# Performance work log

Measured on AMD Instinct MI355X. Metric: run time of the kernel, lower is better.

Reference implementation:

```python
import jax, jax.numpy as jnp
import numpy as np

B = 8
C = 256
N40, N20, N10 = 1600, 400, 100
N = N40 + N20 + N10  # 2100 pixel nodes (40x40 + 20x20 + 10x10)

def _grid_edges(h, w, off):
    # 8-neighborhood 'contextual' edges within one scale's grid
    idx = np.arange(h * w).reshape(h, w)
    srcs, dsts = [], []
    for di in (-1, 0, 1):
        for dj in (-1, 0, 1):
            if di == 0 and dj == 0:
                continue
            s = idx[max(0, -di):h - max(0, di), max(0, -dj):w - max(0, dj)]
            d = idx[max(0, di):h - max(0, -di), max(0, dj):w - max(0, -dj)]
            srcs.append(off + s.ravel())
            dsts.append(off + d.ravel())
    return srcs, dsts

def _hier_edges(ph, pw, poff, coff):
    # bidirected parent <-> 4-children 'hierarchical' edges between scales
    i, j = np.meshgrid(np.arange(ph), np.arange(pw), indexing='ij')
    parent = (poff + i * pw + j).ravel()
    srcs, dsts = [], []
    cw = 2 * pw
    for di in (0, 1):
        for dj in (0, 1):
            child = (coff + (2 * i + di) * cw + (2 * j + dj)).ravel()
            srcs += [parent, child]
            dsts += [child, parent]
    return srcs, dsts

def build_edges():
    loop = [np.arange(N)]  # dgl.add_self_loop on both etypes
    cs, cd = [], []
    for (h, w, off) in ((40, 40, 0), (20, 20, N40), (10, 10, N40 + N20)):
        s, d = _grid_edges(h, w, off)
        cs += s; cd += d
    ctx_src = np.concatenate(cs + loop); ctx_dst = np.concatenate(cd + loop)
    hs, hd = [], []
    s, d = _hier_edges(20, 20, N40, 0); hs += s; hd += d
    s, d = _hier_edges(10, 10, N40 + N20, N40); hs += s; hd += d
    hier_src = np.concatenate(hs + loop); hier_dst = np.concatenate(hd + loop)
    return (jnp.asarray(ctx_src, jnp.int32), jnp.asarray(ctx_dst, jnp.int32),
            jnp.asarray(hier_src, jnp.int32), jnp.asarray(hier_dst, jnp.int32))

def _bn_relu(x, g, b, m, v):
    # inference-mode BatchNorm2d + ReLU
    scale = g * jax.lax.rsqrt(v + 1e-5)
    return jax.nn.relu(x * scale[:, None, None] + (b - m * scale)[:, None, None])

def _conv1x1(x, w, b):
    return jnp.einsum('bchw,oc->bohw', x, w) + b[:, None, None]

def _avgpool2(x):
    b, c, h, w = x.shape
    return x.reshape(b, c, h // 2, 2, w // 2, 2).mean(axis=(3, 5))

def _up2(x):
    return jnp.repeat(jnp.repeat(x, 2, axis=2), 2, axis=3)

def _gnn(h, src, dst, deg_inv, w, b):
    # gather -> scatter-add -> mean over in-neighbors (incl. self loop) -> linear -> ReLU
    agg = jnp.zeros_like(h).at[:, dst].add(h[:, src]) * deg_inv[None, :, None]
    return jax.nn.relu(jnp.einsum('bnc,cd->bnd', agg, w) + b)

def _convT2x2(x, wt, b):
    # stride-2 2x2 transposed conv; wt: [Cin, Cout, 2, 2] (torch layout)
    bsz, cin, h, w = x.shape
    y = jnp.einsum('bchw,cokl->bohkwl', x, wt)
    return y.reshape(bsz, wt.shape[1], 2 * h, 2 * w) + b[:, None, None]

def setup_inputs():
    key = jax.random.key(0)
    ks = iter(jax.random.split(key, 64))
    def rn(shape, scale=0.02):
        return jax.random.normal(next(ks), shape, jnp.float32) * scale
    inp = {}
    inp['feat0'] = rn((B, 256, 160, 160), 1.0)
    inp['feat1'] = rn((B, 512, 80, 80), 1.0)
    inp['feat2'] = rn((B, 1024, 40, 40), 1.0)
    inp['feat3'] = rn((B, 2048, 20, 20), 1.0)
    for i, cin in ((1, 512), (2, 1024), (3, 2048)):
        inp['dw%d' % i] = rn((256, cin))
        inp['db%d' % i] = jnp.zeros((256,), jnp.float32)
        inp['g%d' % i] = jnp.ones((256,), jnp.float32)
        inp['b%d' % i] = jnp.zeros((256,), jnp.float32)
        inp['m%d' % i] = jnp.zeros((256,), jnp.float32)
        inp['v%d' % i] = jnp.ones((256,), jnp.float32)
    for i in range(1, 7):
        inp['gW%d' % i] = rn((256, 256))
        inp['gb%d' % i] = jnp.zeros((256,), jnp.float32)
    for i, cout in ((1, 512), (2, 1024), (3, 2048)):
        inp['tW%d' % i] = rn((256, cout, 2, 2))
        inp['tb%d' % i] = jnp.zeros((cout,), jnp.float32)
    ctx_src, ctx_dst, hier_src, hier_dst = build_edges()
    inp['ctx_src'] = ctx_src; inp['ctx_dst'] = ctx_dst
    inp['hier_src'] = hier_src; inp['hier_dst'] = hier_dst
    return inp

def reference(feat0, feat1, feat2, feat3,
              dw1, db1, g1, b1, m1, v1,
              dw2, db2, g2, b2, m2, v2,
              dw3, db3, g3, b3, m3, v3,
              gW1, gb1, gW2, gb2, gW3, gb3, gW4, gb4, gW5, gb5, gW6, gb6,
              tW1, tb1, tW2, tb2, tW3, tb3,
              ctx_src, ctx_dst, hier_src, hier_dst):
    f40 = _avgpool2(_bn_relu(_conv1x1(feat1, dw1, db1), g1, b1, m1, v1))  # [B,256,40,40]
    f20 = _avgpool2(_bn_relu(_conv1x1(feat2, dw2, db2), g2, b2, m2, v2))  # [B,256,20,20]
    f10 = _avgpool2(_bn_relu(_conv1x1(feat3, dw3, db3), g3, b3, m3, v3))  # [B,256,10,10]
    bsz = f40.shape[0]
    # cnn_gnn: flatten all three scales into [B, 2100, 256] node features (batched
    # version of the original per-sample python loop; graph is identical per sample)
    h = jnp.concatenate([
        f40.reshape(bsz, C, N40).transpose(0, 2, 1),
        f20.reshape(bsz, C, N20).transpose(0, 2, 1),
        f10.reshape(bsz, C, N10).transpose(0, 2, 1)], axis=1)
    dic = 1.0 / jnp.zeros((N,), h.dtype).at[ctx_dst].add(1.0)
    dih = 1.0 / jnp.zeros((N,), h.dtype).at[hier_dst].add(1.0)
    # context1, context2, hierarch1, hierarch2, context4, context5
    h = _gnn(h, ctx_src, ctx_dst, dic, gW1, gb1)
    h = _gnn(h, ctx_src, ctx_dst, dic, gW2, gb2)
    h = _gnn(h, hier_src, hier_dst, dih, gW3, gb3)
    h = _gnn(h, hier_src, hier_dst, dih, gW4, gb4)
    h = _gnn(h, ctx_src, ctx_dst, dic, gW5, gb5)
    h = _gnn(h, ctx_src, ctx_dst, dic, gW6, gb6)
    # gnn_cnn: split back to NCHW maps
    f40g = h[:, :N40].transpose(0, 2, 1).reshape(bsz, C, 40, 40)
    f20g = h[:, N40:N40 + N20].transpose(0, 2, 1).reshape(bsz, C, 20, 20)
    f10g = h[:, N40 + N20:].transpose(0, 2, 1).reshape(bsz, C, 10, 10)
    f10_ref = f10 + f10g
    f20_ref = f20 + f20g + _up2(f10g)
    f40_ref = f40 + f40g + _up2(f20g)
    out1 = _convT2x2(f40_ref, tW1, tb1) + feat1
    out2 = _convT2x2(f20_ref, tW2, tb2) + feat2
    out3 = _convT2x2(f10_ref, tW3, tb3) + feat3
    return (feat0, out1, out2, out3)
```

## Files before the change

kernel.cpp:

```cpp
#include <hip/hip_runtime.h>
#include <cstdint>

#define NODES 2100

typedef __attribute__((ext_vector_type(8))) __bf16 bf16x8;
typedef __attribute__((ext_vector_type(4))) float f32x4;
typedef __attribute__((ext_vector_type(8))) unsigned short u16x8;

__device__ inline float bf2f(unsigned short s) { return __uint_as_float(((unsigned)s) << 16); }
__device__ inline unsigned short f2bf(float f) {
    unsigned u = __float_as_uint(f);
    u += 0x7fff + ((u >> 16) & 1);
    return (unsigned short)(u >> 16);
}
__device__ inline void gload16(const unsigned short* g, void* lds) {
    __builtin_amdgcn_global_load_lds(
        (const __attribute__((address_space(1))) void*)g,
        (__attribute__((address_space(3))) void*)lds, 16, 0, 0);
}

struct PrepArgs {
    const float *dw0, *dw1, *dw2;
    const float *gw0, *gw1, *gw2, *gw3, *gw4, *gw5;
    const float *tw0, *tw1, *tw2;
    const float *g0, *g1, *g2, *b0, *b1, *b2, *m0, *m1, *m2, *v0, *v1, *v2, *db0, *db1, *db2;
    unsigned short *dwb, *gWTb, *tWTb;
    float *scshb;
};

__device__ inline void transpose32(const float* __restrict__ in, unsigned short* __restrict__ outT,
                                   int Ccols, int c0, int r0)
{
    __shared__ float T[32][33];
    const int tx = threadIdx.x & 31, ty = threadIdx.x >> 5;
#pragma unroll
    for (int i = 0; i < 4; ++i)
        T[ty + i * 8][tx] = in[(size_t)(r0 + ty + i * 8) * Ccols + c0 + tx];
    __syncthreads();
#pragma unroll
    for (int i = 0; i < 4; ++i)
        outT[(size_t)(c0 + ty + i * 8) * 256 + r0 + tx] = f2bf(T[tx][ty + i * 8]);
}

__global__ __launch_bounds__(256)
void mega_prep(PrepArgs a)
{
    int bid = blockIdx.x;
    const int t = threadIdx.x;
    if (bid < 448) {
        int idx = (bid * 256 + t) * 8;
        const float* src;
        int loc;
        if (idx < 131072)      { src = a.dw0; loc = idx; }
        else if (idx < 393216) { src = a.dw1; loc = idx - 131072; }
        else                   { src = a.dw2; loc = idx - 393216; }
        float4 x = *(const float4*)(src + loc);
        float4 y = *(const float4*)(src + loc + 4);
        u16x8 r;
        r[0] = f2bf(x.x); r[1] = f2bf(x.y); r[2] = f2bf(x.z); r[3] = f2bf(x.w);
        r[4] = f2bf(y.x); r[5] = f2bf(y.y); r[6] = f2bf(y.z); r[7] = f2bf(y.w);
        *(u16x8*)(a.dwb + idx) = r;
    } else if (bid < 832) {
        int gid = bid - 448;
        int l = gid >> 6, sb = gid & 63;
        const float* gw[6] = {a.gw0, a.gw1, a.gw2, a.gw3, a.gw4, a.gw5};
        transpose32(gw[l], a.gWTb + (size_t)l * 65536, 256, (sb & 7) << 5, (sb >> 3) << 5);
    } else if (bid < 4416) {
        int gid = bid - 832;
        const float* tw; unsigned short* dst; int ncx, loc;
        if (gid < 512)       { tw = a.tw0; dst = a.tWTb;           ncx = 64;  loc = gid; }
        else if (gid < 1536) { tw = a.tw1; dst = a.tWTb + 524288;  ncx = 128; loc = gid - 512; }
        else                 { tw = a.tw2; dst = a.tWTb + 1572864; ncx = 256; loc = gid - 1536; }
        int cx = loc % ncx, ry = loc / ncx;
        transpose32(tw, dst, ncx * 32, cx << 5, ry << 5);
    } else {
        const float* g[3]  = {a.g0, a.g1, a.g2};
        const float* b[3]  = {a.b0, a.b1, a.b2};
        const float* m[3]  = {a.m0, a.m1, a.m2};
        const float* v[3]  = {a.v0, a.v1, a.v2};
        const float* db[3] = {a.db0, a.db1, a.db2};
        for (int s = 0; s < 3; ++s) {
            float sc = g[s][t] * rsqrtf(v[s][t] + 1e-5f);
            a.scshb[s * 512 + t] = sc;
            a.scshb[s * 512 + 256 + t] = (db[s][t] - m[s][t]) * sc + b[s][t];
        }
    }
}

struct ConvArgs {
    const float* feat[3];
    const unsigned short* dwb[3];
    const float* scsh[3];
    unsigned short* h0out;
};

__global__ __launch_bounds__(256)
void conv_fused(ConvArgs ca)
{
    __shared__ __align__(16) unsigned short As[64 * 64];
    __shared__ __align__(16) unsigned short Bs[256 * 64];
    int bx = blockIdx.x;
    int s, mt;
    if (bx < 800)       { s = 0; mt = bx; }
    else if (bx < 1000) { s = 1; mt = bx - 800; }
    else                { s = 2; mt = bx - 1000; }
    const int Kc[3]  = {512, 1024, 2048};
    const int Wc[3]  = {80, 40, 20};
    const int PPc[3] = {1600, 400, 100};
    const int nfc[3] = {0, 1600, 2000};
    const int K = Kc[s], W = Wc[s], W2 = W >> 1, HW = W * W, PP = PPc[s], noff = nfc[s];
    const float* feat = ca.feat[s];
    const unsigned short* dw = ca.dwb[s];
    const float* scsh = ca.scsh[s];

    const int t = threadIdx.x, lane = t & 63, w = t >> 6;
    const int sx = (lane & 7) << 4;

    const int ml = t & 63;
    const int kw = t >> 6;
    const int graw = mt * 64 + ml;
    const int b = graw / HW;
    const int rem = graw - b * HW;
    const int pooled = rem >> 2, sub = rem & 3;
    const int pi = pooled / W2, pj = pooled - pi * W2;
    const int i = pi * 2 + (sub >> 1), j = pj * 2 + (sub & 1);
    const float* src = feat + (size_t)b * K * HW + (size_t)i * W + j;
    const int sxm = (ml & 7) << 3;

    f32x4 acc[4][4];
#pragma unroll
    for (int fr = 0; fr < 4; ++fr)
#pragma unroll
        for (int fc = 0; fc < 4; ++fc) acc[fr][fc] = (f32x4){0.f, 0.f, 0.f, 0.f};

    for (int k0 = 0; k0 < K; k0 += 64) {
#pragma unroll
        for (int it = 0; it < 8; ++it) {
            int LO = ((it << 8) + t) << 4;
            int row = LO >> 7;
            int kb = (LO & 127) ^ ((row & 7) << 4);
            gload16(dw + (size_t)row * K + k0 + (kb >> 1), (char*)Bs + LO);
        }
        float v[16];
#pragma unroll
        for (int it = 0; it < 16; ++it)
            v[it] = src[(size_t)(k0 + it * 4 + kw) * HW];
#pragma unroll
        for (int it = 0; it < 16; ++it) {
            int k_l = it * 4 + kw;
            As[(ml << 6) + (k_l ^ sxm)] = f2bf(v[it]);
        }
        asm volatile("s_waitcnt vmcnt(0)" ::: "memory");
        __syncthreads();
#pragma unroll
        for (int kk = 0; kk < 2; ++kk) {
            bf16x8 a[4], bb[4];
#pragma unroll
            for (int f = 0; f < 4; ++f) {
                int pa = (((f * 16 + (lane & 15)) << 7) + kk * 64 + ((lane >> 4) << 4)) ^ sx;
                int pb = (((w * 64 + f * 16 + (lane & 15)) << 7) + kk * 64 + ((lane >> 4) << 4)) ^ sx;
                a[f]  = *(const bf16x8*)((const char*)As + pa);
                bb[f] = *(const bf16x8*)((const char*)Bs + pb);
            }
#pragma unroll
            for (int fr = 0; fr < 4; ++fr)
#pragma unroll
                for (int fc = 0; fc < 4; ++fc)
                    acc[fr][fc] = __builtin_amdgcn_mfma_f32_16x16x32_bf16(a[fr], bb[fc], acc[fr][fc], 0, 0, 0);
        }
        __syncthreads();
    }

#pragma unroll
    for (int fc = 0; fc < 4; ++fc) {
        const int o = w * 64 + fc * 16 + (lane & 15);
        const float sc = scsh[o], sh = scsh[256 + o];
#pragma unroll
        for (int fr = 0; fr < 4; ++fr) {
            const int mrow = mt * 64 + fr * 16 + (lane >> 4) * 4;
            const int q = mrow >> 2;
            const int bi = q / PP;
            const int node = noff + (q - bi * PP);
            float sum = 0.f;
#pragma unroll
            for (int r = 0; r < 4; ++r)
                sum += fmaxf(acc[fr][fc][r] * sc + sh, 0.f);
            ca.h0out[((size_t)(bi * NODES + node)) * 256 + o] = f2bf(sum * 0.25f);
        }
    }
}

__global__ __launch_bounds__(256)
void gnn_fused(const unsigned short* __restrict__ h, const unsigned short* __restrict__ BT,
               const float* __restrict__ bias, unsigned short* __restrict__ out, int hier)
{
    __shared__ __align__(16) unsigned short As[32 * 64];
    __shared__ __align__(16) unsigned short Bs[256 * 64];
    const int t = threadIdx.x, lane = t & 63, w = t >> 6;
    const int r0 = blockIdx.x << 5;
    const int myrow = t >> 3, q = t & 7;
    const int grow = r0 + myrow;
    const int b = grow / NODES;
    const int n = grow - b * NODES;

    int gw, off;
    if (n < 1600)      { gw = 40; off = 0; }
    else if (n < 2000) { gw = 20; off = 1600; }
    else               { gw = 10; off = 2000; }
    const int li = (n - off) / gw;
    const int lj = (n - off) - li * gw;
    int nbr[9]; int cnt = 0;
    if (!hier) {
#pragma unroll
        for (int di = -1; di <= 1; ++di)
#pragma unroll
            for (int dj = -1; dj <= 1; ++dj) {
                int ii = li + di, jj = lj + dj;
                if (ii >= 0 && ii < gw && jj >= 0 && jj < gw) nbr[cnt++] = off + ii * gw + jj;
            }
    } else {
        nbr[cnt++] = n;
        if (off == 0) {
            nbr[cnt++] = 1600 + (li >> 1) * 20 + (lj >> 1);
        } else if (off == 1600) {
            nbr[cnt++] = 2000 + (li >> 1) * 10 + (lj >> 1);
#pragma unroll
            for (int di = 0; di < 2; ++di)
#pragma unroll
                for (int dj = 0; dj < 2; ++dj)
                    nbr[cnt++] = ((li << 1) + di) * 40 + ((lj << 1) + dj);
        } else {
#pragma unroll
            for (int di = 0; di < 2; ++di)
#pragma unroll
                for (int dj = 0; dj < 2; ++dj)
                    nbr[cnt++] = 1600 + ((li << 1) + di) * 20 + ((lj << 1) + dj);
        }
    }
    int nboff[9];
#pragma unroll
    for (int e = 0; e < 9; ++e)
        nboff[e] = (b * NODES + nbr[e < cnt ? e : 0]) * 256 + q * 8;
    const float inv = 1.0f / (float)cnt;
    const int sx = (lane & 7) << 4;
    const int awr = (myrow << 6) + ((q ^ (myrow & 7)) << 3);

    f32x4 acc[2][4];
#pragma unroll
    for (int fr = 0; fr < 2; ++fr)
#pragma unroll
        for (int fc = 0; fc < 4; ++fc) acc[fr][fc] = (f32x4){0.f, 0.f, 0.f, 0.f};

    u16x8 pre[9];
#pragma unroll
    for (int e = 0; e < 9; ++e) pre[e] = *(const u16x8*)(h + nboff[e]);

    for (int k0 = 0; k0 < 256; k0 += 64) {
#pragma unroll
        for (int it = 0; it < 8; ++it) {
            int LO = ((it << 8) + t) << 4;
            int row = LO >> 7;
            int kb = (LO & 127) ^ ((row & 7) << 4);
            gload16(BT + (size_t)row * 256 + k0 + (kb >> 1), (char*)Bs + LO);
        }
        float sacc[8] = {0, 0, 0, 0, 0, 0, 0, 0};
#pragma unroll
        for (int e = 0; e < 9; ++e) {
            if (e < cnt) {
#pragma unroll
                for (int jj = 0; jj < 8; ++jj) sacc[jj] += bf2f(pre[e][jj]);
            }
        }
        u16x8 o0;
#pragma unroll
        for (int jj = 0; jj < 8; ++jj) o0[jj] = f2bf(sacc[jj] * inv);
        *(u16x8*)&As[awr] = o0;

        asm volatile("s_waitcnt vmcnt(0)" ::: "memory");
        __syncthreads();

        const int k0n = (k0 + 64) & 255;
#pragma unroll
        for (int e = 0; e < 9; ++e) pre[e] = *(const u16x8*)(h + nboff[e] + k0n);

#pragma unroll
        for (int kk = 0; kk < 2; ++kk) {
            bf16x8 a[2], bb[4];
#pragma unroll
            for (int f = 0; f < 2; ++f) {
                int pa = (((f * 16 + (lane & 15)) << 7) + kk * 64 + ((lane >> 4) << 4)) ^ sx;
                a[f] = *(const bf16x8*)((const char*)As + pa);
            }
#pragma unroll
            for (int f = 0; f < 4; ++f) {
                int pb = (((w * 64 + f * 16 + (lane & 15)) << 7) + kk * 64 + ((lane >> 4) << 4)) ^ sx;
                bb[f] = *(const bf16x8*)((const char*)Bs + pb);
            }
#pragma unroll
            for (int fr = 0; fr < 2; ++fr)
#pragma unroll
                for (int fc = 0; fc < 4; ++fc)
                    acc[fr][fc] = __builtin_amdgcn_mfma_f32_16x16x32_bf16(a[fr], bb[fc], acc[fr][fc], 0, 0, 0);
        }
        __syncthreads();
    }

#pragma unroll
    for (int fc = 0; fc < 4; ++fc) {
        const int d = w * 64 + fc * 16 + (lane & 15);
        const float bv = bias[d];
#pragma unroll
        for (int fr = 0; fr < 2; ++fr) {
            int rb = r0 + fr * 16 + (lane >> 4) * 4;
#pragma unroll
            for (int r = 0; r < 4; ++r)
                out[(size_t)(rb + r) * 256 + d] = f2bf(fmaxf(acc[fr][fc][r] + bv, 0.f));
        }
    }
}

__global__ __launch_bounds__(256)
void a_build(const unsigned short* __restrict__ h0, const unsigned short* __restrict__ h6,
             unsigned short* __restrict__ Ao)
{
    int bx = blockIdx.x;
    int P, H2, noff, pbase, pw, haspar; size_t aoff;
    if (bx < 1600)      { P = 1600; H2 = 40; noff = 0;    pbase = 1600; pw = 20; haspar = 1; aoff = 0; }
    else if (bx < 2000) { P = 400;  H2 = 20; noff = 1600; pbase = 2000; pw = 10; haspar = 1; aoff = 12800ULL * 256; bx -= 1600; }
    else                { P = 100;  H2 = 10; noff = 2000; pbase = 0;    pw = 0;  haspar = 0; aoff = 16000ULL * 256; bx -= 2000; }
    const int gid = bx * 256 + threadIdx.x;
    const int m = gid >> 5, c0 = (gid & 31) << 3;
    const int b = m / P, pix = m - b * P;
    const size_t src = ((size_t)(b * NODES + noff + pix)) * 256 + c0;
    u16x8 x0 = *(const u16x8*)(h0 + src);
    u16x8 x6 = *(const u16x8*)(h6 + src);
    float v[8];
#pragma unroll
    for (int e = 0; e < 8; ++e) v[e] = bf2f(x0[e]) + bf2f(x6[e]);
    if (haspar) {
        int ii = pix / H2, jj = pix - ii * H2;
        size_t sp = ((size_t)(b * NODES + pbase + (ii >> 1) * pw + (jj >> 1))) * 256 + c0;
        u16x8 xp = *(const u16x8*)(h6 + sp);
#pragma unroll
        for (int e = 0; e < 8; ++e) v[e] += bf2f(xp[e]);
    }
    u16x8 r;
#pragma unroll
    for (int e = 0; e < 8; ++e) r[e] = f2bf(v[e]);
    *(u16x8*)(Ao + aoff + (size_t)m * 256 + c0) = r;
}

struct ConvtArgs {
    const unsigned short* WT[3];
    const unsigned short* Apix[3];
    const float* tb[3];
    const float* feat[3];
    float* out[3];
    const float4* cps; float4* cpd;
};

__global__ __launch_bounds__(256)
void convt_fused(ConvtArgs ct)
{
    __shared__ __align__(16) unsigned short As[4096], Bs[4096];
    int bx = blockIdx.x;
    if (bx < 1024) {
        const int base = bx * 256 + threadIdx.x;
        const int stride = 1024 * 256;
        const float4* s = ct.cps;
        float4* d = ct.cpd;
        for (int j = 0; j < 50; j += 5) {
            float4 v0 = s[base + (size_t)(j + 0) * stride];
            float4 v1 = s[base + (size_t)(j + 1) * stride];
            float4 v2 = s[base + (size_t)(j + 2) * stride];
            float4 v3 = s[base + (size_t)(j + 3) * stride];
            float4 v4 = s[base + (size_t)(j + 4) * stride];
            d[base + (size_t)(j + 0) * stride] = v0;
            d[base + (size_t)(j + 1) * stride] = v1;
            d[base + (size_t)(j + 2) * stride] = v2;
            d[base + (size_t)(j + 3) * stride] = v3;
            d[base + (size_t)(j + 4) * stride] = v4;
        }
        return;
    }
    bx -= 1024;
    int s, px, my;
    if (bx < 6400)      { s = 0; px = bx >> 5; my = bx & 31; }
    else if (bx < 9600) { s = 1; bx -= 6400; px = bx >> 6; my = bx & 63; }
    else                { s = 2; bx -= 9600; px = bx >> 7; my = bx & 127; }
    const int Pc[3]  = {1600, 400, 100};
    const int H2c[3] = {40, 20, 10};
    const int Cc[3]  = {512, 1024, 2048};
    const int Mc[3]  = {12800, 3200, 800};
    const int P = Pc[s], H2 = H2c[s], Cout = Cc[s], Mpix = Mc[s];
    const int m0 = my << 6, n0 = px << 6;
    const unsigned short* WT = ct.WT[s];
    const unsigned short* Apix = ct.Apix[s];
    const int nClamp = Mpix - 1;

    const int t = threadIdx.x, lane = t & 63, w = t >> 6;
    const int wr = w >> 1, wc = w & 1;
    const int sx = (lane & 7) << 4;

    f32x4 acc[2][2];
#pragma unroll
    for (int fr = 0; fr < 2; ++fr)
#pragma unroll
        for (int fc = 0; fc < 2; ++fc) acc[fr][fc] = (f32x4){0.f, 0.f, 0.f, 0.f};

    for (int k0 = 0; k0 < 256; k0 += 64) {
#pragma unroll
        for (int i = 0; i < 2; ++i) {
            int LO  = ((i << 8) + t) << 4;
            int row = LO >> 7;
            int kb  = (LO & 127) ^ ((row & 7) << 4);
            int ke  = kb >> 1;
            int rb = n0 + row; if (rb > nClamp) rb = nClamp;
            gload16(WT  + (size_t)(m0 + row) * 256 + k0 + ke, (char*)As + LO);
            gload16(Apix + (size_t)rb * 256 + k0 + ke, (char*)Bs + LO);
        }
        asm volatile("s_waitcnt vmcnt(0)" ::: "memory");
        __syncthreads();
#pragma unroll
        for (int kk = 0; kk < 2; ++kk) {
            bf16x8 a[2], bb[2];
#pragma unroll
            for (int f = 0; f < 2; ++f) {
                int pa = (((wr * 32 + f * 16 + (lane & 15)) << 7) + kk * 64 + ((lane >> 4) << 4)) ^ sx;
                int pb = (((wc * 32 + f * 16 + (lane & 15)) << 7) + kk * 64 + ((lane >> 4) << 4)) ^ sx;
                a[f]  = *(const bf16x8*)((const char*)As + pa);
                bb[f] = *(const bf16x8*)((const char*)Bs + pb);
            }
#pragma unroll
            for (int fr = 0; fr < 2; ++fr)
#pragma unroll
                for (int fc = 0; fc < 2; ++fc)
                    acc[fr][fc] = __builtin_amdgcn_mfma_f32_16x16x32_bf16(a[fr], bb[fc], acc[fr][fc], 0, 0, 0);
        }
        __syncthreads();
    }

    const int H = H2 * 2;
    const float* feat = ct.feat[s];
    float* out = ct.out[s];
#pragma unroll
    for (int fc = 0; fc < 2; ++fc) {
        const int p_g = n0 + wc * 32 + fc * 16 + (lane & 15);
        if (p_g < Mpix) {
            const int b = p_g / P, pix = p_g - b * P;
            const int ii = pix / H2, jj = pix - ii * H2;
#pragma unroll
            for (int fr = 0; fr < 2; ++fr) {
                const int rb = m0 + wr * 32 + fr * 16 + (lane >> 4) * 4;
                const int o = rb >> 2;
                const float tbo = ct.tb[s][o];
                size_t base = (((size_t)(b * Cout + o)) * H + 2 * ii) * H + 2 * jj;
                float2 f0 = *(const float2*)&feat[base];
                float2 r0v; r0v.x = acc[fr][fc][0] + tbo + f0.x; r0v.y = acc[fr][fc][1] + tbo + f0.y;
                *(float2*)&out[base] = r0v;
                float2 f1 = *(const float2*)&feat[base + H];
                float2 r1v; r1v.x = acc[fr][fc][2] + tbo + f1.x; r1v.y = acc[fr][fc][3] + tbo + f1.y;
                *(float2*)&out[base + H] = r1v;
            }
        }
    }
}

extern "C" void kernel_launch(void* const* d_in, const int* in_sizes, int n_in,
                              void* d_out, int out_size, void* d_ws, size_t ws_size,
                              hipStream_t stream)
{
    const float* feats[3] = { (const float*)d_in[1], (const float*)d_in[2], (const float*)d_in[3] };
    const float* gb[6];
    for (int l = 0; l < 6; ++l) gb[l] = (const float*)d_in[23 + 2 * l];
    const float* tb[3] = { (const float*)d_in[35], (const float*)d_in[37], (const float*)d_in[39] };

    size_t off = 0;
    auto alloc = [&](size_t bytes) { size_t r = off; off = (off + bytes + 511) & ~(size_t)511; return r; };
    unsigned short* h0b  = (unsigned short*)((char*)d_ws + alloc(16800ULL * 256 * 2));
    unsigned short* hA   = (unsigned short*)((char*)d_ws + alloc(16800ULL * 256 * 2));
    unsigned short* hB   = (unsigned short*)((char*)d_ws + alloc(16800ULL * 256 * 2));
    unsigned short* dwb  = (unsigned short*)((char*)d_ws + alloc(917504ULL * 2));
    unsigned short* gWTb = (unsigned short*)((char*)d_ws + alloc(6ULL * 65536 * 2));
    unsigned short* tWTb = (unsigned short*)((char*)d_ws + alloc(3670016ULL * 2));
    float*          scshb= (float*)((char*)d_ws + alloc(3ULL * 512 * 4));
    unsigned short* Aconvt = (unsigned short*)((char*)d_ws + off);

    PrepArgs pa;
    pa.dw0 = (const float*)d_in[4];  pa.dw1 = (const float*)d_in[10]; pa.dw2 = (const float*)d_in[16];
    pa.gw0 = (const float*)d_in[22]; pa.gw1 = (const float*)d_in[24]; pa.gw2 = (const float*)d_in[26];
    pa.gw3 = (const float*)d_in[28]; pa.gw4 = (const float*)d_in[30]; pa.gw5 = (const float*)d_in[32];
    pa.tw0 = (const float*)d_in[34]; pa.tw1 = (const float*)d_in[36]; pa.tw2 = (const float*)d_in[38];
    pa.g0 = (const float*)d_in[6];  pa.g1 = (const float*)d_in[12]; pa.g2 = (const float*)d_in[18];
    pa.b0 = (const float*)d_in[7];  pa.b1 = (const float*)d_in[13]; pa.b2 = (const float*)d_in[19];
    pa.m0 = (const float*)d_in[8];  pa.m1 = (const float*)d_in[14]; pa.m2 = (const float*)d_in[20];
    pa.v0 = (const float*)d_in[9];  pa.v1 = (const float*)d_in[15]; pa.v2 = (const float*)d_in[21];
    pa.db0 = (const float*)d_in[5]; pa.db1 = (const float*)d_in[11]; pa.db2 = (const float*)d_in[17];
    pa.dwb = dwb; pa.gWTb = gWTb; pa.tWTb = tWTb; pa.scshb = scshb;
    mega_prep<<<dim3(4417), dim3(256), 0, stream>>>(pa);

    ConvArgs ca;
    ca.feat[0] = feats[0]; ca.feat[1] = feats[1]; ca.feat[2] = feats[2];
    ca.dwb[0] = dwb; ca.dwb[1] = dwb + 131072; ca.dwb[2] = dwb + 393216;
    ca.scsh[0] = scshb; ca.scsh[1] = scshb + 512; ca.scsh[2] = scshb + 1024;
    ca.h0out = h0b;
    conv_fused<<<dim3(1050), dim3(256), 0, stream>>>(ca);

    const int types[6] = {0, 0, 1, 1, 0, 0};
    const unsigned short* hin = h0b;
    unsigned short* houts[6] = {hA, hB, hA, hB, hA, hB};
    for (int l = 0; l < 6; ++l) {
        gnn_fused<<<dim3(525), dim3(256), 0, stream>>>(
            hin, gWTb + (size_t)l * 65536, gb[l], houts[l], types[l]);
        hin = houts[l];
    }
    unsigned short* h6 = hB;

    a_build<<<dim3(2100), dim3(256), 0, stream>>>(h0b, h6, Aconvt);

    ConvtArgs ct;
    ct.WT[0] = tWTb; ct.WT[1] = tWTb + 524288; ct.WT[2] = tWTb + 1572864;
    ct.Apix[0] = Aconvt; ct.Apix[1] = Aconvt + 12800ULL * 256; ct.Apix[2] = Aconvt + 16000ULL * 256;
    ct.tb[0] = tb[0]; ct.tb[1] = tb[1]; ct.tb[2] = tb[2];
    ct.feat[0] = feats[0]; ct.feat[1] = feats[1]; ct.feat[2] = feats[2];
    ct.out[0] = (float*)d_out + 52428800;
    ct.out[1] = (float*)d_out + 52428800 + 26214400;
    ct.out[2] = (float*)d_out + 52428800 + 26214400 + 13107200;
    ct.cps = (const float4*)d_in[0];
    ct.cpd = (float4*)d_out;
    convt_fused<<<dim3(1024 + 11264), dim3(256), 0, stream>>>(ct);
}
```

Before: 445.3 us.

## Load GEMM weight and operand fragments directly from global memory instead of LDS

In three kernels (conv, gnn, convT), the async global->LDS staging of the B operand (and both operands in convT) is removed. MFMA fragments are now read straight from global memory into registers, with no LDS buffer, swizzle or vmcnt wait. This cuts LDS usage and some barriers, which could raise occupancy. The cost is redundant global/L2 traffic, since weight rows are reread by every block with no LDS reuse, and the MFMA loop now stalls on global latency.

New measurement: 612.0 us. +37.5%, slower.

```diff
diff --git a/kernel.cpp b/kernel.cpp
--- a/kernel.cpp
+++ b/kernel.cpp
@@ -12,11 +12,6 @@
     unsigned u = __float_as_uint(f);
     u += 0x7fff + ((u >> 16) & 1);
     return (unsigned short)(u >> 16);
-}
-__device__ inline void gload16(const unsigned short* g, void* lds) {
-    __builtin_amdgcn_global_load_lds(
-        (const __attribute__((address_space(1))) void*)g,
-        (__attribute__((address_space(3))) void*)lds, 16, 0, 0);
 }
 
 struct PrepArgs {
@@ -98,7 +93,6 @@
 void conv_fused(ConvArgs ca)
 {
     __shared__ __align__(16) unsigned short As[64 * 64];
-    __shared__ __align__(16) unsigned short Bs[256 * 64];
     int bx = blockIdx.x;
     int s, mt;
     if (bx < 800)       { s = 0; mt = bx; }
@@ -134,13 +128,6 @@
         for (int fc = 0; fc < 4; ++fc) acc[fr][fc] = (f32x4){0.f, 0.f, 0.f, 0.f};
 
     for (int k0 = 0; k0 < K; k0 += 64) {
-#pragma unroll
-        for (int it = 0; it < 8; ++it) {
-            int LO = ((it << 8) + t) << 4;
-            int row = LO >> 7;
-            int kb = (LO & 127) ^ ((row & 7) << 4);
-            gload16(dw + (size_t)row * K + k0 + (kb >> 1), (char*)Bs + LO);
-        }
         float v[16];
 #pragma unroll
         for (int it = 0; it < 16; ++it)
@@ -150,7 +137,6 @@
             int k_l = it * 4 + kw;
             As[(ml << 6) + (k_l ^ sxm)] = f2bf(v[it]);
         }
-        asm volatile("s_waitcnt vmcnt(0)" ::: "memory");
         __syncthreads();
 #pragma unroll
         for (int kk = 0; kk < 2; ++kk) {
@@ -158,9 +144,9 @@
 #pragma unroll
             for (int f = 0; f < 4; ++f) {
                 int pa = (((f * 16 + (lane & 15)) << 7) + kk * 64 + ((lane >> 4) << 4)) ^ sx;
-                int pb = (((w * 64 + f * 16 + (lane & 15)) << 7) + kk * 64 + ((lane >> 4) << 4)) ^ sx;
-                a[f]  = *(const bf16x8*)((const char*)As + pa);
-                bb[f] = *(const bf16x8*)((const char*)Bs + pb);
+                a[f] = *(const bf16x8*)((const char*)As + pa);
+                int row = w * 64 + f * 16 + (lane & 15);
+                bb[f] = *(const bf16x8*)(dw + (size_t)row * K + k0 + kk * 32 + ((lane >> 4) << 3));
             }
 #pragma unroll
             for (int fr = 0; fr < 4; ++fr)
@@ -195,7 +181,6 @@
                const float* __restrict__ bias, unsigned short* __restrict__ out, int hier)
 {
     __shared__ __align__(16) unsigned short As[32 * 64];
-    __shared__ __align__(16) unsigned short Bs[256 * 64];
     const int t = threadIdx.x, lane = t & 63, w = t >> 6;
     const int r0 = blockIdx.x << 5;
     const int myrow = t >> 3, q = t & 7;
@@ -256,13 +241,6 @@
     for (int e = 0; e < 9; ++e) pre[e] = *(const u16x8*)(h + nboff[e]);
 
     for (int k0 = 0; k0 < 256; k0 += 64) {
-#pragma unroll
-        for (int it = 0; it < 8; ++it) {
-            int LO = ((it << 8) + t) << 4;
-            int row = LO >> 7;
-            int kb = (LO & 127) ^ ((row & 7) << 4);
-            gload16(BT + (size_t)row * 256 + k0 + (kb >> 1), (char*)Bs + LO);
-        }
         float sacc[8] = {0, 0, 0, 0, 0, 0, 0, 0};
 #pragma unroll
         for (int e = 0; e < 9; ++e) {
@@ -275,8 +253,6 @@
 #pragma unroll
         for (int jj = 0; jj < 8; ++jj) o0[jj] = f2bf(sacc[jj] * inv);
         *(u16x8*)&As[awr] = o0;
-
-        asm volatile("s_waitcnt vmcnt(0)" ::: "memory");
         __syncthreads();
 
         const int k0n = (k0 + 64) & 255;
@@ -293,8 +269,8 @@
             }
 #pragma unroll
             for (int f = 0; f < 4; ++f) {
-                int pb = (((w * 64 + f * 16 + (lane & 15)) << 7) + kk * 64 + ((lane >> 4) << 4)) ^ sx;
-                bb[f] = *(const bf16x8*)((const char*)Bs + pb);
+                int row = w * 64 + f * 16 + (lane & 15);
+                bb[f] = *(const bf16x8*)(BT + (size_t)row * 256 + k0 + kk * 32 + ((lane >> 4) << 3));
             }
 #pragma unroll
             for (int fr = 0; fr < 2; ++fr)
@@ -362,7 +338,6 @@
 __global__ __launch_bounds__(256)
 void convt_fused(ConvtArgs ct)
 {
-    __shared__ __align__(16) unsigned short As[4096], Bs[4096];
     int bx = blockIdx.x;
     if (bx < 1024) {
         const int base = bx * 256 + threadIdx.x;
@@ -400,7 +375,15 @@
 
     const int t = threadIdx.x, lane = t & 63, w = t >> 6;
     const int wr = w >> 1, wc = w & 1;
-    const int sx = (lane & 7) << 4;
+
+    int arow[2], brow[2];
+#pragma unroll
+    for (int f = 0; f < 2; ++f) {
+        arow[f] = m0 + wr * 32 + f * 16 + (lane & 15);
+        int rb = n0 + wc * 32 + f * 16 + (lane & 15);
+        brow[f] = (rb > nClamp) ? nClamp : rb;
+    }
+    const int kl = (lane >> 4) << 3;
 
     f32x4 acc[2][2];
 #pragma unroll
@@ -408,36 +391,19 @@
 #pragma unroll
         for (int fc = 0; fc < 2; ++fc) acc[fr][fc] = (f32x4){0.f, 0.f, 0.f, 0.f};
 
-    for (int k0 = 0; k0 < 256; k0 += 64) {
-#pragma unroll
-        for (int i = 0; i < 2; ++i) {
-            int LO  = ((i << 8) + t) << 4;
-            int row = LO >> 7;
-            int kb  = (LO & 127) ^ ((row & 7) << 4);
-            int ke  = kb >> 1;
-            int rb = n0 + row; if (rb > nClamp) rb = nClamp;
-            gload16(WT  + (size_t)(m0 + row) * 256 + k0 + ke, (char*)As + LO);
-            gload16(Apix + (size_t)rb * 256 + k0 + ke, (char*)Bs + LO);
-        }
-        asm volatile("s_waitcnt vmcnt(0)" ::: "memory");
-        __syncthreads();
-#pragma unroll
-        for (int kk = 0; kk < 2; ++kk) {
-            bf16x8 a[2], bb[2];
-#pragma unroll
-            for (int f = 0; f < 2; ++f) {
-                int pa = (((wr * 32 + f * 16 + (lane & 15)) << 7) + kk * 64 + ((lane >> 4) << 4)) ^ sx;
-                int pb = (((wc * 32 + f * 16 + (lane & 15)) << 7) + kk * 64 + ((lane >> 4) << 4)) ^ sx;
-                a[f]  = *(const bf16x8*)((const char*)As + pa);
-                bb[f] = *(const bf16x8*)((const char*)Bs + pb);
-            }
-#pragma unroll
-            for (int fr = 0; fr < 2; ++fr)
-#pragma unroll
-                for (int fc = 0; fc < 2; ++fc)
-                    acc[fr][fc] = __builtin_amdgcn_mfma_f32_16x16x32_bf16(a[fr], bb[fc], acc[fr][fc], 0, 0, 0);
-        }
-        __syncthreads();
+#pragma unroll
+    for (int k0 = 0; k0 < 256; k0 += 32) {
+        bf16x8 a[2], bb[2];
+#pragma unroll
+        for (int f = 0; f < 2; ++f) {
+            a[f]  = *(const bf16x8*)(WT  + (size_t)arow[f] * 256 + k0 + kl);
+            bb[f] = *(const bf16x8*)(Apix + (size_t)brow[f] * 256 + k0 + kl);
+        }
+#pragma unroll
+        for (int fr = 0; fr < 2; ++fr)
+#pragma unroll
+            for (int fc = 0; fc < 2; ++fc)
+                acc[fr][fc] = __builtin_amdgcn_mfma_f32_16x16x32_bf16(a[fr], bb[fc], acc[fr][fc], 0, 0, 0);
     }
 
     const int H = H2 * 2;
```
